# Performance work log

Hardware: AMD Instinct MI355X
Metric: run time of the kernel (lower is better)

Reference implementation:

```python
import jax, jax.numpy as jnp
import numpy as np

D_MODEL = 1024
NUM_HEADS = 16
HEAD_DIM = D_MODEL // NUM_HEADS


def setup_inputs() -> dict:
    key = jax.random.key(0)
    ks = jax.random.split(key, 11)
    B, S = 2, 2048
    s = 1.0 / np.sqrt(D_MODEL)
    inp = {
        "query": jax.random.normal(ks[0], (B, S, D_MODEL), jnp.float32),
        "key": jax.random.normal(ks[1], (B, S, D_MODEL), jnp.float32),
        "value": jax.random.normal(ks[2], (B, S, D_MODEL), jnp.float32),
        "Wq": jax.random.normal(ks[3], (D_MODEL, D_MODEL), jnp.float32) * s,
        "bq": jnp.zeros((D_MODEL,), jnp.float32),
        "Wk": jax.random.normal(ks[4], (D_MODEL, D_MODEL), jnp.float32) * s,
        "bk": jnp.zeros((D_MODEL,), jnp.float32),
        "Wv": jax.random.normal(ks[5], (D_MODEL, D_MODEL), jnp.float32) * s,
        "bv": jnp.zeros((D_MODEL,), jnp.float32),
        "Wo": jax.random.normal(ks[6], (D_MODEL, D_MODEL), jnp.float32) * s,
        "bo": jnp.zeros((D_MODEL,), jnp.float32),
    }
    return inp


def _split_heads(x):
    B, S, _ = x.shape
    return x.reshape(B, S, NUM_HEADS, HEAD_DIM).transpose(0, 2, 1, 3)  # [B,H,S,d]


def reference(query, key, value, Wq, bq, Wk, bk, Wv, bv, Wo, bo):
    Q = _split_heads(query @ Wq.T + bq)
    K = _split_heads(key @ Wk.T + bk)
    V = _split_heads(value @ Wv.T + bv)
    scale = 1.0 / jnp.sqrt(jnp.asarray(HEAD_DIM, jnp.float32))
    scores = jnp.einsum("bhqd,bhkd->bhqk", Q, K) * scale  # [B,H,S,S]
    weights = jax.nn.softmax(scores, axis=-1)
    attn = jnp.einsum("bhqk,bhkd->bhqd", weights, V)
    B, H, S, d = attn.shape
    attn = attn.transpose(0, 2, 1, 3).reshape(B, S, H * d)
    return attn @ Wo.T + bo
```

## Files before the change

kernel.cpp:

```cpp
#include <hip/hip_runtime.h>
#include <hip/hip_bf16.h>


typedef unsigned short u16;
typedef __attribute__((ext_vector_type(8))) short short8;
typedef __attribute__((ext_vector_type(4))) float floatx4;

__device__ __forceinline__ float bf2f(u16 x) {
  return __uint_as_float(((unsigned)x) << 16);
}
__device__ __forceinline__ u16 f2bf(float f) {
  unsigned x = __float_as_uint(f);
  return (u16)((x + 0x7fffu + ((x >> 16) & 1u)) >> 16);
}
__device__ __forceinline__ ushort2 pk_bf16(float a, float b) {
  __hip_bfloat162 h2 = __float22bfloat162_rn(make_float2(a, b));
  ushort2 u;
  __builtin_memcpy(&u, &h2, 4);
  return u;
}
#if __has_builtin(__builtin_amdgcn_exp2f)
#define EXP2(x) __builtin_amdgcn_exp2f(x)
#else
#define EXP2(x) exp2f(x)
#endif
__device__ __forceinline__ void gll16(const u16* g, u16* lds) {
  __builtin_amdgcn_global_load_lds((const __attribute__((address_space(1))) void*)g,
                                   (__attribute__((address_space(3))) void*)lds,
                                   16, 0, 0);
}

__global__ __launch_bounds__(256) void cvt_kernel(
    const float* __restrict__ q, const float* __restrict__ k, const float* __restrict__ v,
    const float* __restrict__ wq, const float* __restrict__ wk,
    const float* __restrict__ wv, const float* __restrict__ wo,
    const float* __restrict__ bq, const float* __restrict__ bk,
    const float* __restrict__ bv, const float* __restrict__ bo,
    u16* __restrict__ ws) {
  const int i4 = (blockIdx.x * 256 + threadIdx.x) * 4;
  const float* src;
  u16* dst;
  int local;
  if (i4 < 4194304)        { src = q;  dst = ws;            local = i4; }
  else if (i4 < 8388608)   { src = k;  dst = ws + 4194304;  local = i4 - 4194304; }
  else if (i4 < 12582912)  { src = v;  dst = ws + 8388608;  local = i4 - 8388608; }
  else if (i4 < 13631488)  { src = wq; dst = ws + 12582912; local = i4 - 12582912; }
  else if (i4 < 14680064)  { src = wk; dst = ws + 13631488; local = i4 - 13631488; }
  else if (i4 < 15728640)  { src = wv; dst = ws + 14680064; local = i4 - 14680064; }
  else if (i4 < 16777216)  { src = wo; dst = ws + 15728640; local = i4 - 15728640; }
  else if (i4 < 16778240)  { src = bq; dst = ws + 16777216; local = i4 - 16777216; }
  else if (i4 < 16779264)  { src = bk; dst = ws + 16779264; local = i4 - 16778240; }
  else if (i4 < 16780288)  { src = bv; dst = ws + 16781312; local = i4 - 16779264; }
  else                     { src = bo; dst = ws + 16783360; local = i4 - 16780288; }
  const float4 f = *(const float4*)(src + local);
  ushort4 o;
  o.x = f2bf(f.x); o.y = f2bf(f.y); o.z = f2bf(f.z); o.w = f2bf(f.w);
  *(ushort4*)(dst + local) = o;
}

template <int MTILE>
__device__ __forceinline__ void gemm_tile(
    const u16* __restrict__ X, const u16* __restrict__ W,
    const u16* __restrict__ bias, u16* __restrict__ out16, float* __restrict__ out32,
    int row0, int col0, int mode, float oscale, u16* As, u16* Bs) {
  constexpr int NI = MTILE / 32;
  constexpr int ABUF = MTILE * 32;
  const int tid = threadIdx.x;
  const int w = tid >> 6, l = tid & 63;
  const int lan = l & 15, quad = l >> 4;
  const int wm = w & 1, wn = w >> 1;

  floatx4 acc[NI][4];
#pragma unroll
  for (int i = 0; i < NI; ++i)
#pragma unroll
    for (int j = 0; j < 4; ++j) acc[i][j] = (floatx4)0.0f;

  const int r0 = tid >> 2, kq0 = tid & 3;
  const int r1 = (tid + 256) >> 2;
  const int woff = w * 512;
  const u16* Xa0 = X + (size_t)(row0 + r0) * 1024 + kq0 * 8;
  const u16* Xa1 = X + (size_t)(row0 + (MTILE == 128 ? r1 : r0)) * 1024 + kq0 * 8;
  const u16* Wb0 = W + (size_t)(col0 + r0) * 1024 + kq0 * 8;
  const u16* Wb1 = W + (size_t)(col0 + r1) * 1024 + kq0 * 8;

#define STAGE(buf, kt)                                           \
  do {                                                           \
    gll16(Xa0 + (kt) * 32, As + (buf) * ABUF + woff);            \
    if (MTILE == 128)                                            \
      gll16(Xa1 + (kt) * 32, As + (buf) * ABUF + 2048 + woff);   \
    gll16(Wb0 + (kt) * 32, Bs + (buf) * 4096 + woff);            \
    gll16(Wb1 + (kt) * 32, Bs + (buf) * 4096 + 2048 + woff);     \
  } while (0)

  STAGE(0, 0);
  int cur = 0;
  for (int kt = 0; kt < 32; ++kt) {
    if (kt < 31) {
      const int nb = cur == 2 ? 0 : cur + 1;
      STAGE(nb, kt + 1);
      if (MTILE == 128)
        __asm__ volatile("s_waitcnt vmcnt(4)" ::: "memory");
      else
        __asm__ volatile("s_waitcnt vmcnt(3)" ::: "memory");
    } else {
      __asm__ volatile("s_waitcnt vmcnt(0)" ::: "memory");
    }
    __builtin_amdgcn_s_barrier();

    const u16* Ab = As + cur * ABUF;
    const u16* Bb = Bs + cur * 4096;
    short8 af[NI], bfr[4];
#pragma unroll
    for (int i = 0; i < NI; ++i)
      af[i] = *(const short8*)(Ab + (wm * (MTILE / 2) + i * 16 + lan) * 32 + quad * 8);
#pragma unroll
    for (int j = 0; j < 4; ++j)
      bfr[j] = *(const short8*)(Bb + (wn * 64 + j * 16 + lan) * 32 + quad * 8);
#pragma unroll
    for (int i = 0; i < NI; ++i)
#pragma unroll
      for (int j = 0; j < 4; ++j)
        acc[i][j] = __builtin_amdgcn_mfma_f32_16x16x32_bf16(af[i], bfr[j], acc[i][j], 0, 0, 0);
    cur = cur == 2 ? 0 : cur + 1;
  }
#undef STAGE

#pragma unroll
  for (int i = 0; i < NI; ++i) {
    const int mb = row0 + wm * (MTILE / 2) + i * 16 + quad * 4;
#pragma unroll
    for (int j = 0; j < 4; ++j) {
      const int n = col0 + wn * 64 + j * 16 + lan;
      const float bv = bf2f(bias[n]);
      if (mode == 0) {
#pragma unroll
        for (int r = 0; r < 4; ++r)
          out16[(size_t)(mb + r) * 1024 + n] = f2bf((acc[i][j][r] + bv) * oscale);
      } else if (mode == 1) {
        const int b = mb >> 11;
        const int h = n >> 6, dd = n & 63;
        u16* base = out16 + (size_t)((b * 16 + h) * 64 + dd) * 2048;
        const int s0 = mb & 2047;
        const int k0 = s0 & 63;
        const int sp0 = (s0 & ~63) | (((k0 >> 4) & 1) << 5) | (((k0 >> 2) & 3) << 3) |
                        (((k0 >> 5) & 1) << 2);
        ushort4 ov;
        ov.x = f2bf(acc[i][j][0] + bv);
        ov.y = f2bf(acc[i][j][1] + bv);
        ov.z = f2bf(acc[i][j][2] + bv);
        ov.w = f2bf(acc[i][j][3] + bv);
        *(ushort4*)(base + sp0) = ov;
      } else {
#pragma unroll
        for (int r = 0; r < 4; ++r)
          out32[(size_t)(mb + r) * 1024 + n] = acc[i][j][r] + bv;
      }
    }
  }
}

__global__ __launch_bounds__(256) void qkv_kernel(
    const u16* __restrict__ xq, const u16* __restrict__ xk, const u16* __restrict__ xv,
    const u16* __restrict__ Wq, const u16* __restrict__ Wk, const u16* __restrict__ Wv,
    const u16* __restrict__ bq, const u16* __restrict__ bk, const u16* __restrict__ bv,
    u16* __restrict__ Qo, u16* __restrict__ Ko, u16* __restrict__ Vto) {
  __shared__ __align__(16) u16 As[3 * 4096];
  __shared__ __align__(16) u16 Bs[3 * 4096];
  const int bx = blockIdx.x;
  const int xcd = bx & 7;
  const int j = bx >> 3;
  const int c = j & 7;
  const int gidx = j >> 3;
  const int g = gidx * 8 + xcd;
  const int which = g >> 5;
  const int tile_m = g & 31;
  const int col0 = c * 128;
  const u16* X = which == 0 ? xq : (which == 1 ? xk : xv);
  const u16* W = which == 0 ? Wq : (which == 1 ? Wk : Wv);
  const u16* bias = which == 0 ? bq : (which == 1 ? bk : bv);
  u16* out = which == 0 ? Qo : (which == 1 ? Ko : Vto);
  const float C = 0.125f * 1.4426950408889634f;
  gemm_tile<128>(X, W, bias, out, nullptr, tile_m * 128, col0, which == 2 ? 1 : 0,
                 which == 0 ? C : 1.0f, As, Bs);
}

__global__ __launch_bounds__(256) void proj_kernel(
    const u16* __restrict__ X, const u16* __restrict__ W,
    const u16* __restrict__ bias, float* __restrict__ out) {
  __shared__ __align__(16) u16 As[3 * 2048];
  __shared__ __align__(16) u16 Bs[3 * 4096];
  const int bx = blockIdx.x;
  const int xcd = bx & 7;
  const int j = bx >> 3;
  const int c = j & 7;
  const int gidx = j >> 3;
  const int tm = xcd * 8 + gidx;
  gemm_tile<64>(X, W, bias, nullptr, out, tm * 64, c * 128, 2, 1.0f, As, Bs);
}

#define FIXMAX 16.0f
#define KPAD 72
__global__ __launch_bounds__(256, 2) void attn_kernel(
    const u16* __restrict__ Q, const u16* __restrict__ K,
    const u16* __restrict__ Vt, u16* __restrict__ O) {
  __shared__ __align__(16) u16 Ks[2][64 * KPAD];
  __shared__ __align__(16) u16 Vs[2][64 * KPAD];
  const int tid = threadIdx.x;
  const int w = tid >> 6, l = tid & 63;
  const int lan = l & 15, quad = l >> 4;
  const int id = blockIdx.x + (blockIdx.y << 4);
  const int xcd = id & 7;
  const int jj = id >> 3;
  const int bh = xcd * 4 + (jj >> 4);
  const int q0 = (jj & 15) * 128;
  const int b = bh >> 4, h = bh & 15;
  const u16* Qg = Q + (size_t)(b * 2048 + q0) * 1024 + h * 64;
  const u16* Kg = K + (size_t)(b * 2048) * 1024 + h * 64;
  const u16* Vg = Vt + (size_t)((b * 16 + h) * 64) * 2048;

  short8 qf[2][2];
#pragma unroll
  for (int mi = 0; mi < 2; ++mi)
#pragma unroll
    for (int kk = 0; kk < 2; ++kk)
      qf[mi][kk] = *(const short8*)(Qg + (size_t)(w * 32 + mi * 16 + lan) * 1024 +
                                    kk * 32 + quad * 8);

  float lrun[2] = {0.f, 0.f};
  floatx4 oacc[2][4];
#pragma unroll
  for (int mi = 0; mi < 2; ++mi)
#pragma unroll
    for (int nd = 0; nd < 4; ++nd) oacc[mi][nd] = (floatx4)0.0f;

  const int rowA = tid >> 3, colq = (tid & 7) * 8;
  const int rowB = rowA + 32;

  short8 k0 = *(const short8*)(Kg + (size_t)rowA * 1024 + colq);
  short8 k1 = *(const short8*)(Kg + (size_t)rowB * 1024 + colq);
  short8 v0 = *(const short8*)(Vg + (size_t)rowA * 2048 + colq);
  short8 v1 = *(const short8*)(Vg + (size_t)rowB * 2048 + colq);
  *(short8*)(Ks[0] + rowA * KPAD + colq) = k0;
  *(short8*)(Ks[0] + rowB * KPAD + colq) = k1;
  *(short8*)(Vs[0] + rowA * KPAD + colq) = v0;
  *(short8*)(Vs[0] + rowB * KPAD + colq) = v1;
  __syncthreads();

  for (int kt = 0; kt < 32; ++kt) {
    const int cur = kt & 1;
    if (kt < 31) {
      const int kn = kt + 1;
      k0 = *(const short8*)(Kg + (size_t)(kn * 64 + rowA) * 1024 + colq);
      k1 = *(const short8*)(Kg + (size_t)(kn * 64 + rowB) * 1024 + colq);
      v0 = *(const short8*)(Vg + (size_t)rowA * 2048 + kn * 64 + colq);
      v1 = *(const short8*)(Vg + (size_t)rowB * 2048 + kn * 64 + colq);
    }
    const u16* Kc = Ks[cur];
    const u16* Vc = Vs[cur];

    short8 kf[4][2];
#pragma unroll
    for (int nj = 0; nj < 4; ++nj)
#pragma unroll
      for (int kk = 0; kk < 2; ++kk)
        kf[nj][kk] = *(const short8*)(Kc + (nj * 16 + lan) * KPAD + kk * 32 + quad * 8);

    floatx4 sacc[2][4];
#pragma unroll
    for (int mi = 0; mi < 2; ++mi)
#pragma unroll
      for (int nj = 0; nj < 4; ++nj) sacc[mi][nj] = (floatx4)(-FIXMAX);
    __builtin_amdgcn_s_setprio(1);
#pragma unroll
    for (int kk = 0; kk < 2; ++kk)
#pragma unroll
      for (int mi = 0; mi < 2; ++mi)
#pragma unroll
        for (int nj = 0; nj < 4; ++nj)
          sacc[mi][nj] =
              __builtin_amdgcn_mfma_f32_16x16x32_bf16(kf[nj][kk], qf[mi][kk], sacc[mi][nj], 0, 0, 0);
    __builtin_amdgcn_s_setprio(0);

    short8 vf[4][2];
#pragma unroll
    for (int nd = 0; nd < 4; ++nd)
#pragma unroll
      for (int kk = 0; kk < 2; ++kk)
        vf[nd][kk] = *(const short8*)(Vc + (nd * 16 + lan) * KPAD + kk * 32 + quad * 8);

    short8 pb[2][2];
#pragma unroll
    for (int mi = 0; mi < 2; ++mi) {
      float p[4][4];
#pragma unroll
      for (int nj = 0; nj < 4; ++nj)
#pragma unroll
        for (int r = 0; r < 4; ++r) p[nj][r] = EXP2(sacc[mi][nj][r]);
      float s01 = 0.f, s23 = 0.f;
#pragma unroll
      for (int r = 0; r < 4; ++r) {
        s01 += p[0][r] + p[1][r];
        s23 += p[2][r] + p[3][r];
      }
      lrun[mi] += s01 + s23;
#pragma unroll
      for (int kk = 0; kk < 2; ++kk) {
        const ushort2 w0 = pk_bf16(p[kk][0], p[kk][1]);
        const ushort2 w1 = pk_bf16(p[kk][2], p[kk][3]);
        const ushort2 w2 = pk_bf16(p[kk + 2][0], p[kk + 2][1]);
        const ushort2 w3 = pk_bf16(p[kk + 2][2], p[kk + 2][3]);
        union { short8 s8; ushort us[8]; } u;
        u.us[0] = w0.x; u.us[1] = w0.y; u.us[2] = w1.x; u.us[3] = w1.y;
        u.us[4] = w2.x; u.us[5] = w2.y; u.us[6] = w3.x; u.us[7] = w3.y;
        pb[mi][kk] = u.s8;
      }
    }

    __builtin_amdgcn_s_setprio(1);
#pragma unroll
    for (int kk = 0; kk < 2; ++kk)
#pragma unroll
      for (int mi = 0; mi < 2; ++mi)
#pragma unroll
        for (int nd = 0; nd < 4; ++nd)
          oacc[mi][nd] =
              __builtin_amdgcn_mfma_f32_16x16x32_bf16(vf[nd][kk], pb[mi][kk], oacc[mi][nd], 0, 0, 0);
    __builtin_amdgcn_s_setprio(0);

    if (kt < 31) {
      u16* Kn = Ks[cur ^ 1];
      u16* Vn = Vs[cur ^ 1];
      *(short8*)(Kn + rowA * KPAD + colq) = k0;
      *(short8*)(Kn + rowB * KPAD + colq) = k1;
      *(short8*)(Vn + rowA * KPAD + colq) = v0;
      *(short8*)(Vn + rowB * KPAD + colq) = v1;
      __syncthreads();
    }
  }

#pragma unroll
  for (int mi = 0; mi < 2; ++mi) {
    float ls = lrun[mi];
    ls += __shfl_xor(ls, 16);
    ls += __shfl_xor(ls, 32);
    const float inv = 1.0f / ls;
    const int qg = b * 2048 + q0 + w * 32 + mi * 16 + lan;
#pragma unroll
    for (int nd = 0; nd < 4; ++nd) {
      ushort4 ov;
      ov.x = f2bf(oacc[mi][nd][0] * inv);
      ov.y = f2bf(oacc[mi][nd][1] * inv);
      ov.z = f2bf(oacc[mi][nd][2] * inv);
      ov.w = f2bf(oacc[mi][nd][3] * inv);
      *(ushort4*)(O + (size_t)qg * 1024 + h * 64 + nd * 16 + quad * 4) = ov;
    }
  }
}

extern "C" void kernel_launch(void* const* d_in, const int* in_sizes, int n_in,
                              void* d_out, int out_size, void* d_ws, size_t ws_size,
                              hipStream_t stream) {
  const float* query = (const float*)d_in[0];
  const float* key_ = (const float*)d_in[1];
  const float* value = (const float*)d_in[2];
  const float* Wq = (const float*)d_in[3];
  const float* bq = (const float*)d_in[4];
  const float* Wk = (const float*)d_in[5];
  const float* bk = (const float*)d_in[6];
  const float* Wv = (const float*)d_in[7];
  const float* bv = (const float*)d_in[8];
  const float* Wo = (const float*)d_in[9];
  const float* bo = (const float*)d_in[10];
  float* out = (float*)d_out;

  u16* ws = (u16*)d_ws;
  u16* Xq = ws;
  u16* Xk = ws + 4194304;
  u16* Xv = ws + 8388608;
  u16* cWq = ws + 12582912;
  u16* cWk = ws + 13631488;
  u16* cWv = ws + 14680064;
  u16* cWo = ws + 15728640;
  u16* cbq = ws + 16777216;
  u16* cbk = ws + 16779264;
  u16* cbv = ws + 16781312;
  u16* cbo = ws + 16783360;
  u16* Qw = ws + 17301504;
  u16* Kw = ws + 21495808;
  u16* Vtw = ws + 25690112;
  u16* Ow = ws + 29884416;

  cvt_kernel<<<16388, 256, 0, stream>>>(query, key_, value, Wq, Wk, Wv, Wo,
                                        bq, bk, bv, bo, ws);
  qkv_kernel<<<768, 256, 0, stream>>>(Xq, Xk, Xv, cWq, cWk, cWv, cbq, cbk, cbv,
                                      Qw, Kw, Vtw);
  attn_kernel<<<dim3(16, 32), 256, 0, stream>>>(Qw, Kw, Vtw, Ow);
  proj_kernel<<<512, 256, 0, stream>>>(Ow, cWo, cbo, out);
}
```

Before: 218.7 us.

## Split KV tiles across wave pairs in attention, each wave covering 64 query rows

Restructures the attention kernel so each pair of waves shares 64 query rows, and the two waves alternate processing even and odd KV tiles. Each wave now does a 64x64 score tile per step, which raises MFMA work per LDS fragment load. Partial outputs and row sums are combined through shared memory at the end. This halves per-wave tile count but doubles register accumulators (oacc 4x4) and idles half the waves each iteration, with the risk of register pressure or lost latency hiding.

```diff
diff --git a/kernel.cpp b/kernel.cpp
--- a/kernel.cpp
+++ b/kernel.cpp
@@ -204,11 +204,12 @@
 __global__ __launch_bounds__(256, 2) void attn_kernel(
     const u16* __restrict__ Q, const u16* __restrict__ K,
     const u16* __restrict__ Vt, u16* __restrict__ O) {
-  __shared__ __align__(16) u16 Ks[2][64 * KPAD];
-  __shared__ __align__(16) u16 Vs[2][64 * KPAD];
+  __shared__ __align__(16) u16 KV[4][64 * KPAD];
   const int tid = threadIdx.x;
   const int w = tid >> 6, l = tid & 63;
   const int lan = l & 15, quad = l >> 4;
+  const int g = w >> 1;
+  const int par = w & 1;
   const int id = blockIdx.x + (blockIdx.y << 4);
   const int xcd = id & 7;
   const int jj = id >> 3;
@@ -219,18 +220,18 @@
   const u16* Kg = K + (size_t)(b * 2048) * 1024 + h * 64;
   const u16* Vg = Vt + (size_t)((b * 16 + h) * 64) * 2048;
 
-  short8 qf[2][2];
-#pragma unroll
-  for (int mi = 0; mi < 2; ++mi)
+  short8 qf[4][2];
+#pragma unroll
+  for (int mi = 0; mi < 4; ++mi)
 #pragma unroll
     for (int kk = 0; kk < 2; ++kk)
-      qf[mi][kk] = *(const short8*)(Qg + (size_t)(w * 32 + mi * 16 + lan) * 1024 +
+      qf[mi][kk] = *(const short8*)(Qg + (size_t)(g * 64 + mi * 16 + lan) * 1024 +
                                     kk * 32 + quad * 8);
 
-  float lrun[2] = {0.f, 0.f};
-  floatx4 oacc[2][4];
-#pragma unroll
-  for (int mi = 0; mi < 2; ++mi)
+  float lrun[4] = {0.f, 0.f, 0.f, 0.f};
+  floatx4 oacc[4][4];
+#pragma unroll
+  for (int mi = 0; mi < 4; ++mi)
 #pragma unroll
     for (int nd = 0; nd < 4; ++nd) oacc[mi][nd] = (floatx4)0.0f;
 
@@ -241,10 +242,10 @@
   short8 k1 = *(const short8*)(Kg + (size_t)rowB * 1024 + colq);
   short8 v0 = *(const short8*)(Vg + (size_t)rowA * 2048 + colq);
   short8 v1 = *(const short8*)(Vg + (size_t)rowB * 2048 + colq);
-  *(short8*)(Ks[0] + rowA * KPAD + colq) = k0;
-  *(short8*)(Ks[0] + rowB * KPAD + colq) = k1;
-  *(short8*)(Vs[0] + rowA * KPAD + colq) = v0;
-  *(short8*)(Vs[0] + rowB * KPAD + colq) = v1;
+  *(short8*)(KV[0] + rowA * KPAD + colq) = k0;
+  *(short8*)(KV[0] + rowB * KPAD + colq) = k1;
+  *(short8*)(KV[2] + rowA * KPAD + colq) = v0;
+  *(short8*)(KV[2] + rowB * KPAD + colq) = v1;
   __syncthreads();
 
   for (int kt = 0; kt < 32; ++kt) {
@@ -256,104 +257,127 @@
       v0 = *(const short8*)(Vg + (size_t)rowA * 2048 + kn * 64 + colq);
       v1 = *(const short8*)(Vg + (size_t)rowB * 2048 + kn * 64 + colq);
     }
-    const u16* Kc = Ks[cur];
-    const u16* Vc = Vs[cur];
-
-    short8 kf[4][2];
-#pragma unroll
-    for (int nj = 0; nj < 4; ++nj)
-#pragma unroll
-      for (int kk = 0; kk < 2; ++kk)
-        kf[nj][kk] = *(const short8*)(Kc + (nj * 16 + lan) * KPAD + kk * 32 + quad * 8);
-
-    floatx4 sacc[2][4];
-#pragma unroll
-    for (int mi = 0; mi < 2; ++mi)
-#pragma unroll
-      for (int nj = 0; nj < 4; ++nj) sacc[mi][nj] = (floatx4)(-FIXMAX);
-    __builtin_amdgcn_s_setprio(1);
-#pragma unroll
-    for (int kk = 0; kk < 2; ++kk)
-#pragma unroll
-      for (int mi = 0; mi < 2; ++mi)
+
+    if ((kt & 1) == par) {
+      const u16* Kc = KV[cur];
+      const u16* Vc = KV[2 + cur];
+
+      floatx4 sacc[4][4];
+#pragma unroll
+      for (int mi = 0; mi < 4; ++mi)
+#pragma unroll
+        for (int nj = 0; nj < 4; ++nj) sacc[mi][nj] = (floatx4)(-FIXMAX);
+#pragma unroll
+      for (int kk = 0; kk < 2; ++kk) {
+        short8 kf[4];
 #pragma unroll
         for (int nj = 0; nj < 4; ++nj)
-          sacc[mi][nj] =
-              __builtin_amdgcn_mfma_f32_16x16x32_bf16(kf[nj][kk], qf[mi][kk], sacc[mi][nj], 0, 0, 0);
-    __builtin_amdgcn_s_setprio(0);
-
-    short8 vf[4][2];
-#pragma unroll
-    for (int nd = 0; nd < 4; ++nd)
-#pragma unroll
-      for (int kk = 0; kk < 2; ++kk)
-        vf[nd][kk] = *(const short8*)(Vc + (nd * 16 + lan) * KPAD + kk * 32 + quad * 8);
-
-    short8 pb[2][2];
-#pragma unroll
-    for (int mi = 0; mi < 2; ++mi) {
-      float p[4][4];
-#pragma unroll
-      for (int nj = 0; nj < 4; ++nj)
-#pragma unroll
-        for (int r = 0; r < 4; ++r) p[nj][r] = EXP2(sacc[mi][nj][r]);
-      float s01 = 0.f, s23 = 0.f;
-#pragma unroll
-      for (int r = 0; r < 4; ++r) {
-        s01 += p[0][r] + p[1][r];
-        s23 += p[2][r] + p[3][r];
-      }
-      lrun[mi] += s01 + s23;
+          kf[nj] = *(const short8*)(Kc + (nj * 16 + lan) * KPAD + kk * 32 + quad * 8);
+        __builtin_amdgcn_s_setprio(1);
+#pragma unroll
+        for (int mi = 0; mi < 4; ++mi)
+#pragma unroll
+          for (int nj = 0; nj < 4; ++nj)
+            sacc[mi][nj] = __builtin_amdgcn_mfma_f32_16x16x32_bf16(
+                kf[nj], qf[mi][kk], sacc[mi][nj], 0, 0, 0);
+        __builtin_amdgcn_s_setprio(0);
+      }
+
+      short8 pb[4][2];
+#pragma unroll
+      for (int mi = 0; mi < 4; ++mi) {
+        float p[4][4];
+#pragma unroll
+        for (int nj = 0; nj < 4; ++nj)
+#pragma unroll
+          for (int r = 0; r < 4; ++r) p[nj][r] = EXP2(sacc[mi][nj][r]);
+        float s01 = 0.f, s23 = 0.f;
+#pragma unroll
+        for (int r = 0; r < 4; ++r) {
+          s01 += p[0][r] + p[1][r];
+          s23 += p[2][r] + p[3][r];
+        }
+        lrun[mi] += s01 + s23;
+#pragma unroll
+        for (int kk = 0; kk < 2; ++kk) {
+          const ushort2 w0 = pk_bf16(p[kk][0], p[kk][1]);
+          const ushort2 w1 = pk_bf16(p[kk][2], p[kk][3]);
+          const ushort2 w2 = pk_bf16(p[kk + 2][0], p[kk + 2][1]);
+          const ushort2 w3 = pk_bf16(p[kk + 2][2], p[kk + 2][3]);
+          union { short8 s8; ushort us[8]; } u;
+          u.us[0] = w0.x; u.us[1] = w0.y; u.us[2] = w1.x; u.us[3] = w1.y;
+          u.us[4] = w2.x; u.us[5] = w2.y; u.us[6] = w3.x; u.us[7] = w3.y;
+          pb[mi][kk] = u.s8;
+        }
+      }
+
 #pragma unroll
       for (int kk = 0; kk < 2; ++kk) {
-        const ushort2 w0 = pk_bf16(p[kk][0], p[kk][1]);
-        const ushort2 w1 = pk_bf16(p[kk][2], p[kk][3]);
-        const ushort2 w2 = pk_bf16(p[kk + 2][0], p[kk + 2][1]);
-        const ushort2 w3 = pk_bf16(p[kk + 2][2], p[kk + 2][3]);
-        union { short8 s8; ushort us[8]; } u;
-        u.us[0] = w0.x; u.us[1] = w0.y; u.us[2] = w1.x; u.us[3] = w1.y;
-        u.us[4] = w2.x; u.us[5] = w2.y; u.us[6] = w3.x; u.us[7] = w3.y;
-        pb[mi][kk] = u.s8;
-      }
-    }
-
-    __builtin_amdgcn_s_setprio(1);
-#pragma unroll
-    for (int kk = 0; kk < 2; ++kk)
-#pragma unroll
-      for (int mi = 0; mi < 2; ++mi)
+        short8 vf[4];
 #pragma unroll
         for (int nd = 0; nd < 4; ++nd)
-          oacc[mi][nd] =
-              __builtin_amdgcn_mfma_f32_16x16x32_bf16(vf[nd][kk], pb[mi][kk], oacc[mi][nd], 0, 0, 0);
-    __builtin_amdgcn_s_setprio(0);
+          vf[nd] = *(const short8*)(Vc + (nd * 16 + lan) * KPAD + kk * 32 + quad * 8);
+        __builtin_amdgcn_s_setprio(1);
+#pragma unroll
+        for (int mi = 0; mi < 4; ++mi)
+#pragma unroll
+          for (int nd = 0; nd < 4; ++nd)
+            oacc[mi][nd] = __builtin_amdgcn_mfma_f32_16x16x32_bf16(
+                vf[nd], pb[mi][kk], oacc[mi][nd], 0, 0, 0);
+        __builtin_amdgcn_s_setprio(0);
+      }
+    }
 
     if (kt < 31) {
-      u16* Kn = Ks[cur ^ 1];
-      u16* Vn = Vs[cur ^ 1];
-      *(short8*)(Kn + rowA * KPAD + colq) = k0;
-      *(short8*)(Kn + rowB * KPAD + colq) = k1;
-      *(short8*)(Vn + rowA * KPAD + colq) = v0;
-      *(short8*)(Vn + rowB * KPAD + colq) = v1;
+      const int nxt = cur ^ 1;
+      *(short8*)(KV[nxt] + rowA * KPAD + colq) = k0;
+      *(short8*)(KV[nxt] + rowB * KPAD + colq) = k1;
+      *(short8*)(KV[2 + nxt] + rowA * KPAD + colq) = v0;
+      *(short8*)(KV[2 + nxt] + rowB * KPAD + colq) = v1;
       __syncthreads();
     }
   }
 
 #pragma unroll
-  for (int mi = 0; mi < 2; ++mi) {
-    float ls = lrun[mi];
-    ls += __shfl_xor(ls, 16);
-    ls += __shfl_xor(ls, 32);
-    const float inv = 1.0f / ls;
-    const int qg = b * 2048 + q0 + w * 32 + mi * 16 + lan;
-#pragma unroll
-    for (int nd = 0; nd < 4; ++nd) {
-      ushort4 ov;
-      ov.x = f2bf(oacc[mi][nd][0] * inv);
-      ov.y = f2bf(oacc[mi][nd][1] * inv);
-      ov.z = f2bf(oacc[mi][nd][2] * inv);
-      ov.w = f2bf(oacc[mi][nd][3] * inv);
-      *(ushort4*)(O + (size_t)qg * 1024 + h * 64 + nd * 16 + quad * 4) = ov;
+  for (int mi = 0; mi < 4; ++mi) {
+    lrun[mi] += __shfl_xor(lrun[mi], 16);
+    lrun[mi] += __shfl_xor(lrun[mi], 32);
+  }
+  __syncthreads();
+  float4* obuf = (float4*)&KV[0][0];
+  float* lbuf = (float*)&KV[0][0] + 8192;
+  if (par == 1) {
+#pragma unroll
+    for (int mi = 0; mi < 4; ++mi) {
+#pragma unroll
+      for (int nd = 0; nd < 4; ++nd) {
+        const int fi = mi * 4 + nd;
+        float4 t;
+        t.x = oacc[mi][nd][0]; t.y = oacc[mi][nd][1];
+        t.z = oacc[mi][nd][2]; t.w = oacc[mi][nd][3];
+        obuf[(g * 64 + l) * 16 + ((fi + l) & 15)] = t;
+      }
+      lbuf[(g * 64 + l) * 4 + mi] = lrun[mi];
+    }
+  }
+  __syncthreads();
+  if (par == 0) {
+#pragma unroll
+    for (int mi = 0; mi < 4; ++mi) {
+      const float lt = lrun[mi] + lbuf[(g * 64 + l) * 4 + mi];
+      const float inv = 1.0f / lt;
+      const int qg = b * 2048 + q0 + g * 64 + mi * 16 + lan;
+#pragma unroll
+      for (int nd = 0; nd < 4; ++nd) {
+        const int fi = mi * 4 + nd;
+        const float4 t = obuf[(g * 64 + l) * 16 + ((fi + l) & 15)];
+        ushort4 ov;
+        ov.x = f2bf((oacc[mi][nd][0] + t.x) * inv);
+        ov.y = f2bf((oacc[mi][nd][1] + t.y) * inv);
+        ov.z = f2bf((oacc[mi][nd][2] + t.z) * inv);
+        ov.w = f2bf((oacc[mi][nd][3] + t.w) * inv);
+        *(ushort4*)(O + (size_t)qg * 1024 + h * 64 + nd * 16 + quad * 4) = ov;
+      }
     }
   }
 }
```

New measurement: 222.1 us. No clear change (+1.5%).
